# Kernel optimization log

Measured on AMD Instinct MI355X. Metric: run time of the kernel, lower is better.

Reference implementation:

```python
import jax, jax.numpy as jnp
import numpy as np

N = 100000      # nodes
E = 1600000     # edges (avg degree 16)
IN_C = 128
HID = 64
OUT_C = 2


def compute_norm(edge_index, n):
    """1/rowcount of M = I + A^T (distinct nonzeros per row, coalesce semantics)."""
    idt = edge_index.dtype
    ar = jnp.arange(n, dtype=idt)
    rows = jnp.concatenate([ar, edge_index[1]])  # M built from transposed edges
    cols = jnp.concatenate([ar, edge_index[0]])
    order = jnp.lexsort((cols, rows))
    rs, cs = rows[order], cols[order]
    uniq = jnp.concatenate([jnp.array([True]),
                            (rs[1:] != rs[:-1]) | (cs[1:] != cs[:-1])])
    rowcount = jnp.zeros((n,), jnp.float32).at[rs].add(uniq.astype(jnp.float32))
    return 1.0 / jnp.maximum(rowcount, 1.0)


def pan_conv(x, edge_index, w_lin, b_lin, w_pan, norm):
    # PyG PANConv, filter_size=1: out = diag(norm) @ (w0*I + w0*w1*A^T) @ (x W + b)
    h = x @ w_lin + b_lin                                   # [N, HID]
    src, dst = edge_index[0], edge_index[1]
    agg = jnp.zeros_like(h).at[dst].add(h[src])             # (A^T h)[i] = sum_{src->i} h[src]
    out = w_pan[0] * h + (w_pan[0] * w_pan[1]) * agg
    return norm[:, None] * out


def setup_inputs() -> dict:
    key = jax.random.key(0)
    ks = jax.random.split(key, 8)
    x = jax.random.normal(ks[0], (N, IN_C), jnp.float32)
    edge_index = jax.random.randint(ks[1], (2, E), 0, N, dtype=jnp.int32)
    w1_lin = jax.random.normal(ks[2], (IN_C, HID), jnp.float32) * 0.05
    b1_lin = jnp.zeros((HID,), jnp.float32)
    w1_pan = jax.random.uniform(ks[3], (2,), jnp.float32, 0.5, 1.5)
    w2_lin = jax.random.normal(ks[4], (HID, HID), jnp.float32) * 0.05
    b2_lin = jnp.zeros((HID,), jnp.float32)
    w2_pan = jax.random.uniform(ks[5], (2,), jnp.float32, 0.5, 1.5)
    wc = jax.random.normal(ks[6], (2 * HID, OUT_C), jnp.float32) * 0.05
    bc = jnp.zeros((OUT_C,), jnp.float32)
    return {"x": x, "edge_index": edge_index,
            "w1_lin": w1_lin, "b1_lin": b1_lin, "w1_pan": w1_pan,
            "w2_lin": w2_lin, "b2_lin": b2_lin, "w2_pan": w2_pan,
            "wc": wc, "bc": bc}


def reference(x, edge_index, w1_lin, b1_lin, w1_pan, w2_lin, b2_lin, w2_pan, wc, bc):
    n = x.shape[0]
    norm = compute_norm(edge_index, n)          # graph-structure only; shared by both layers
    h = pan_conv(x, edge_index, w1_lin, b1_lin, w1_pan, norm)
    h = jax.nn.relu(h)
    h = pan_conv(h, edge_index, w2_lin, b2_lin, w2_pan, norm)
    row, col = edge_index[0], edge_index[1]
    emb = jnp.concatenate([h[row], h[col]], axis=-1)  # [E, 2*HID]
    return emb @ wc + bc                               # [E, OUT_C]
```

## Files before the change

### kernel.cpp

```cpp
#include <hip/hip_runtime.h>
#include <hip/hip_bf16.h>

#define NNODES 100000
#define NEDGES 1600000
#define INC 128
#define HIDC 64
#define BSHIFT 7
#define NB ((NNODES + 127) / 128)
#define TILE 4096
#define HSLOTS 4096
#define CAP 4096
#define CAPE 4096
#define NBLK_FILL ((NEDGES + TILE - 1) / TILE)
#define NBLK_LIN ((NNODES + 63) / 64)

typedef short bf16x8 __attribute__((ext_vector_type(8)));
typedef float f32x4 __attribute__((ext_vector_type(4)));

__device__ __forceinline__ float bf2f(unsigned short h) {
    return __uint_as_float((unsigned)h << 16);
}
__device__ __forceinline__ unsigned short f2bf(float f) {
    __hip_bfloat16 h = __float2bfloat16(f);
    return *(unsigned short*)&h;
}

__global__ __launch_bounds__(256) void prep_w_kernel(
        const float* __restrict__ w1, unsigned short* __restrict__ wTh,
        unsigned short* __restrict__ wTl,
        const float* __restrict__ w2_lin, const float* __restrict__ b2,
        const float* __restrict__ wc, float* __restrict__ w44,
        float* __restrict__ bias4, unsigned short* __restrict__ out) {
    int t = threadIdx.x;
    int e = blockIdx.x * 256 + t;
    int c = e >> 7, k = e & 127;
    float v = w1[k * 64 + c];
    unsigned short hi = f2bf(v);
    wTh[e] = hi;
    wTl[e] = f2bf(v - bf2f(hi));
    if (blockIdx.x == 0) {
        if (t < 16)
            *(ushort4*)(out + (size_t)NNODES * 64 + t * 4) = make_ushort4(0, 0, 0, 0);
        int kk = t >> 2, j = t & 3;
        float a = 0.0f;
#pragma unroll 8
        for (int i = 0; i < 64; i++) {
            float w4 = (j < 2) ? wc[i * 2 + j] : wc[(64 + i) * 2 + (j - 2)];
            a += w2_lin[kk * 64 + i] * w4;
        }
        w44[kk * 4 + j] = a;
        if (kk == 0) {
            float bb4 = 0.0f;
            for (int i = 0; i < 64; i++) {
                float w4 = (j < 2) ? wc[i * 2 + j] : wc[(64 + i) * 2 + (j - 2)];
                bb4 += b2[i] * w4;
            }
            bias4[j] = bb4;
        }
    }
}

__global__ __launch_bounds__(256) void fat_kernel(
        const float* __restrict__ x,
        const unsigned short* __restrict__ wTh, const unsigned short* __restrict__ wTl,
        const float* __restrict__ b, unsigned short* __restrict__ out,
        const int* __restrict__ src, const int* __restrict__ dst,
        int* __restrict__ bucket_fill, unsigned int* __restrict__ staging) {
    __shared__ alignas(16) unsigned short s_a[2][64 * 128];
    __shared__ alignas(16) unsigned short s_b[2][64 * 128];
    int t = threadIdx.x;
    if (blockIdx.x < NBLK_FILL) {
        int* cnt = (int*)&s_a[0][0];
        int* basepos = cnt + NB;
        unsigned int* svl = (unsigned int*)&s_b[0][0];
        for (int i = t; i < NB; i += 256) cnt[i] = 0;
        __syncthreads();
        int tile0 = blockIdx.x * TILE;
        int meta[16];
#pragma unroll
        for (int i = 0; i < 16; i++) {
            int e = tile0 + i * 256 + t;
            meta[i] = -1;
            if (e < NEDGES) {
                int s = src[e], d = dst[e];
                int bkt = d >> BSHIFT;
                int r = atomicAdd(&cnt[bkt], 1);
                meta[i] = (bkt << 12) | r;
                svl[i * 256 + t] = ((unsigned)(d & 127) << 17) | (unsigned)s;
            }
        }
        __syncthreads();
        for (int i = t; i < NB; i += 256) {
            int c = cnt[i];
            int g = (c > 0) ? atomicAdd(&bucket_fill[i], c) : 0;
            basepos[i] = (i << 12) + g;
        }
        __syncthreads();
#pragma unroll
        for (int i = 0; i < 16; i++) {
            if (meta[i] >= 0) {
                int bkt = meta[i] >> 12, r = meta[i] & 4095;
                staging[basepos[bkt] + r] = svl[i * 256 + t];
            }
        }
    } else {
        int node0 = (blockIdx.x - NBLK_FILL) * 64;
        float4 vx[8];
#pragma unroll
        for (int it = 0; it < 8; it++) {
            int idx = it * 256 + t;
            int row = idx >> 5, c4 = idx & 31;
            int node = node0 + row;
            if (node < NNODES)
                vx[it] = *(const float4*)(x + (size_t)node * INC + c4 * 4);
            else
                vx[it] = make_float4(0.f, 0.f, 0.f, 0.f);
        }
        uint4 vwh[4], vwl[4];
#pragma unroll
        for (int j = 0; j < 4; j++) {
            vwh[j] = *(const uint4*)(wTh + (size_t)(j * 256 + t) * 8);
            vwl[j] = *(const uint4*)(wTl + (size_t)(j * 256 + t) * 8);
        }
#pragma unroll
        for (int it = 0; it < 8; it++) {
            int idx = it * 256 + t;
            int row = idx >> 5, c4 = idx & 31;
            ushort4 hi, lo;
            hi.x = f2bf(vx[it].x); lo.x = f2bf(vx[it].x - bf2f(hi.x));
            hi.y = f2bf(vx[it].y); lo.y = f2bf(vx[it].y - bf2f(hi.y));
            hi.z = f2bf(vx[it].z); lo.z = f2bf(vx[it].z - bf2f(hi.z));
            hi.w = f2bf(vx[it].w); lo.w = f2bf(vx[it].w - bf2f(hi.w));
            int ke = (c4 * 4) ^ ((row & 7) << 3);
            *(ushort4*)&s_a[0][row * 128 + ke] = hi;
            *(ushort4*)&s_a[1][row * 128 + ke] = lo;
        }
#pragma unroll
        for (int j = 0; j < 4; j++) {
            int idx = j * 256 + t;
            int col = idx >> 4, k0 = (idx & 15) * 8;
            int ke = k0 ^ ((col & 7) << 3);
            *(uint4*)&s_b[0][col * 128 + ke] = vwh[j];
            *(uint4*)&s_b[1][col * 128 + ke] = vwl[j];
        }
        __syncthreads();
        int l = t & 63, wv = t >> 6;
        int mr = l & 15, g = l >> 4;
        int arow = wv * 16 + mr;
        f32x4 acc[4] = {{0.f, 0.f, 0.f, 0.f}, {0.f, 0.f, 0.f, 0.f},
                        {0.f, 0.f, 0.f, 0.f}, {0.f, 0.f, 0.f, 0.f}};
#pragma unroll
        for (int ks = 0; ks < 4; ks++) {
            int k0 = ks * 32 + g * 8;
            int ko = k0 ^ ((mr & 7) << 3);
            bf16x8 ah = *(const bf16x8*)&s_a[0][arow * 128 + ko];
            bf16x8 al = *(const bf16x8*)&s_a[1][arow * 128 + ko];
#pragma unroll
            for (int cb = 0; cb < 4; cb++) {
                int bo = (cb * 16 + mr) * 128 + ko;
                bf16x8 bh = *(const bf16x8*)&s_b[0][bo];
                bf16x8 bl = *(const bf16x8*)&s_b[1][bo];
                acc[cb] = __builtin_amdgcn_mfma_f32_16x16x32_bf16(ah, bh, acc[cb], 0, 0, 0);
                acc[cb] = __builtin_amdgcn_mfma_f32_16x16x32_bf16(ah, bl, acc[cb], 0, 0, 0);
                acc[cb] = __builtin_amdgcn_mfma_f32_16x16x32_bf16(al, bh, acc[cb], 0, 0, 0);
            }
        }
#pragma unroll
        for (int cb = 0; cb < 4; cb++) {
            int col = cb * 16 + mr;
            float bb = b[col];
#pragma unroll
            for (int r = 0; r < 4; r++) {
                int node = node0 + wv * 16 + g * 4 + r;
                if (node < NNODES)
                    out[(size_t)node * 64 + col] = f2bf(acc[cb][r] + bb);
            }
        }
    }
}

__global__ __launch_bounds__(256) void fill2_kernel(
        const int* __restrict__ bucket_fill, const unsigned int* __restrict__ staging,
        int* __restrict__ csr_src, int* __restrict__ row_start,
        int* __restrict__ row_pdeg, float* __restrict__ norm, int n_nodes) {
    __shared__ int cnt[128];
    __shared__ int dcount[128];
    __shared__ int off[128];
    __shared__ int pscan[128];
    __shared__ unsigned short rank16[CAP];
    __shared__ unsigned int ht[HSLOTS];
    int t = threadIdx.x;
    int b = blockIdx.x;
    int node0 = b << BSHIFT;
    int nn = min(128, n_nodes - node0);
    if (t < 128) { cnt[t] = 0; dcount[t] = 0; }
    {
        uint4* h4 = (uint4*)ht;
        uint4 ff = make_uint4(0xFFFFFFFFu, 0xFFFFFFFFu, 0xFFFFFFFFu, 0xFFFFFFFFu);
        for (int i = t; i < HSLOTS / 4; i += 256) h4[i] = ff;
    }
    __syncthreads();
    int start = b << 12;
    int total = bucket_fill[b];
    for (int li = t; li < total; li += 256) {
        unsigned int w = staging[start + li];
        int s = (int)(w & 0x1FFFFu);
        int dl = (int)(w >> 17);
        int r = atomicAdd(&cnt[dl], 1);
        rank16[li] = (unsigned short)r;
        if (s != node0 + dl) {
            unsigned int slot = ((w * 2654435761u) >> 13) & (HSLOTS - 1);
            while (true) {
                unsigned int prev = atomicCAS(&ht[slot], 0xFFFFFFFFu, w);
                if (prev == 0xFFFFFFFFu) { atomicAdd(&dcount[dl], 1); break; }
                if (prev == w) break;
                slot = (slot + 1) & (HSLOTS - 1);
            }
        }
    }
    __syncthreads();
    int cv = 0, pv = 0;
    if (t < 128) {
        cv = cnt[t];
        pv = (cv + 7) & ~7;
        pscan[t] = pv;
    }
    __syncthreads();
    for (int o = 1; o < 128; o <<= 1) {
        int xx = (t >= o && t < 128) ? pscan[t - o] : 0;
        __syncthreads();
        if (t < 128) pscan[t] += xx;
        __syncthreads();
    }
    if (t < 128) off[t] = b * CAPE + pscan[t] - pv;
    __syncthreads();
    if (t < nn) {
        row_start[node0 + t] = off[t];
        row_pdeg[node0 + t] = pv;
        norm[node0 + t] = 1.0f / (1.0f + (float)dcount[t]);
    }
    if (t < 128)
        for (int k = cv; k < pv; k++) csr_src[off[t] + k] = n_nodes << 7;
    for (int li = t; li < total; li += 256) {
        unsigned int w = staging[start + li];
        int s = (int)(w & 0x1FFFFu);
        int dl = (int)(w >> 17);
        csr_src[off[dl] + (int)rank16[li]] = s << 7;
    }
}

__global__ void agg_h_kernel(const unsigned int* __restrict__ lin32,
                             const int* __restrict__ row_start,
                             const int* __restrict__ row_pdeg,
                             const int* __restrict__ csr_src,
                             const float* __restrict__ norm,
                             const float* __restrict__ wpan, const float* __restrict__ w44,
                             const float* __restrict__ bias4, float* __restrict__ u,
                             int n_nodes) {
    int t = threadIdx.x;
    int lane = t & 63;
    int sl = lane & 31;
    int h5 = lane >> 5;
    int quad = blockIdx.x * 4 + (t >> 6);
    if (blockIdx.x == 0 && t < 4) u[n_nodes * 4 + t] = 0.0f;
    int nX = quad * 4 + h5 * 2;
    int nY = nX + 1;
    int e0X = row_start[nX], pdX = row_pdeg[nX];
    int e0Y = row_start[nY], pdY = row_pdeg[nY];
    int pm = max(pdX, pdY);
    int pmax = max(pm, __shfl_xor(pm, 32));
    int sentB = n_nodes << 7;
    unsigned sl4 = (unsigned)sl * 4;
    const char* base8 = (const char*)lin32;
    float xL0 = 0.f, xH0 = 0.f, xL1 = 0.f, xH1 = 0.f;
    float yL0 = 0.f, yH0 = 0.f, yL1 = 0.f, yH1 = 0.f;
    for (int base = 0; base < pmax; base += 32) {
        int li = base + sl;
        int soX = (li < pdX) ? csr_src[e0X + li] : sentB;
        int soY = (li < pdY) ? csr_src[e0Y + li] : sentB;
        int m = min(32, pmax - base);
#pragma unroll
        for (int i = 0; i < 32; i += 2) {
            if (i < m) {
                int xA0 = __builtin_amdgcn_readlane(soX, i);
                int xB0 = __builtin_amdgcn_readlane(soX, 32 + i);
                int xA1 = __builtin_amdgcn_readlane(soX, i + 1);
                int xB1 = __builtin_amdgcn_readlane(soX, 33 + i);
                int yA0 = __builtin_amdgcn_readlane(soY, i);
                int yB0 = __builtin_amdgcn_readlane(soY, 32 + i);
                int yA1 = __builtin_amdgcn_readlane(soY, i + 1);
                int yB1 = __builtin_amdgcn_readlane(soY, 33 + i);
                int ox0 = h5 ? xB0 : xA0;
                int ox1 = h5 ? xB1 : xA1;
                int oy0 = h5 ? yB0 : yA0;
                int oy1 = h5 ? yB1 : yA1;
                unsigned int wx0 = *(const unsigned int*)(base8 + (unsigned)(ox0 + sl4));
                unsigned int wx1 = *(const unsigned int*)(base8 + (unsigned)(ox1 + sl4));
                unsigned int wy0 = *(const unsigned int*)(base8 + (unsigned)(oy0 + sl4));
                unsigned int wy1 = *(const unsigned int*)(base8 + (unsigned)(oy1 + sl4));
                xL0 += __uint_as_float(wx0 << 16);
                xH0 += __uint_as_float(wx0 & 0xFFFF0000u);
                xL1 += __uint_as_float(wx1 << 16);
                xH1 += __uint_as_float(wx1 & 0xFFFF0000u);
                yL0 += __uint_as_float(wy0 << 16);
                yH0 += __uint_as_float(wy0 & 0xFFFF0000u);
                yL1 += __uint_as_float(wy1 << 16);
                yH1 += __uint_as_float(wy1 & 0xFFFF0000u);
            }
        }
    }
    float aLX = xL0 + xL1, aHX = xH0 + xH1;
    float aLY = yL0 + yL1, aHY = yH0 + yH1;
    unsigned int wsX = *(const unsigned int*)(base8 + (unsigned)((nX << 7) + sl4));
    unsigned int wsY = *(const unsigned int*)(base8 + (unsigned)((nY << 7) + sl4));
    float nrX = norm[nX], nrY = norm[nY];
    float w0 = wpan[0];
    float w01 = wpan[0] * wpan[1];
    float vLX = fmaxf(nrX * (w0 * __uint_as_float(wsX << 16) + w01 * aLX), 0.0f);
    float vHX = fmaxf(nrX * (w0 * __uint_as_float(wsX & 0xFFFF0000u) + w01 * aHX), 0.0f);
    float vLY = fmaxf(nrY * (w0 * __uint_as_float(wsY << 16) + w01 * aLY), 0.0f);
    float vHY = fmaxf(nrY * (w0 * __uint_as_float(wsY & 0xFFFF0000u) + w01 * aHY), 0.0f);
    int c0 = 2 * sl;
    float4 wv0 = *(const float4*)(w44 + c0 * 4);
    float4 wv1 = *(const float4*)(w44 + (c0 + 1) * 4);
    float pX0 = vLX * wv0.x + vHX * wv1.x;
    float pX1 = vLX * wv0.y + vHX * wv1.y;
    float pX2 = vLX * wv0.z + vHX * wv1.z;
    float pX3 = vLX * wv0.w + vHX * wv1.w;
    float pY0 = vLY * wv0.x + vHY * wv1.x;
    float pY1 = vLY * wv0.y + vHY * wv1.y;
    float pY2 = vLY * wv0.z + vHY * wv1.z;
    float pY3 = vLY * wv0.w + vHY * wv1.w;
    for (int off = 16; off; off >>= 1) {
        pX0 += __shfl_xor(pX0, off);
        pX1 += __shfl_xor(pX1, off);
        pX2 += __shfl_xor(pX2, off);
        pX3 += __shfl_xor(pX3, off);
        pY0 += __shfl_xor(pY0, off);
        pY1 += __shfl_xor(pY1, off);
        pY2 += __shfl_xor(pY2, off);
        pY3 += __shfl_xor(pY3, off);
    }
    if (sl == 0) {
        float4 bb = *(const float4*)bias4;
        *(float4*)(u + nX * 4) =
            make_float4(pX0 + bb.x, pX1 + bb.y, pX2 + bb.z, pX3 + bb.w);
    }
    if (sl == 1) {
        float4 bb = *(const float4*)bias4;
        *(float4*)(u + nY * 4) =
            make_float4(pY0 + bb.x, pY1 + bb.y, pY2 + bb.z, pY3 + bb.w);
    }
}

__global__ void agg_pq4_kernel(const float* __restrict__ u, const int* __restrict__ row_start,
                               const int* __restrict__ row_pdeg,
                               const int* __restrict__ csr_src,
                               const float* __restrict__ norm,
                               const float* __restrict__ wpan, float* __restrict__ pq,
                               int n_nodes) {
    int t = threadIdx.x;
    int node = blockIdx.x * 64 + (t >> 2);
    int j = t & 3;
    if (node >= n_nodes) return;
    int e0 = row_start[node];
    int pd = row_pdeg[node];
    float acc = 0.0f;
    for (int e = 0; e < pd; e += 8) {
#pragma unroll
        for (int k = 0; k < 8; k++) {
            int so = csr_src[e0 + e + k];
            acc += u[(so >> 5) + j];
        }
    }
    float w0 = wpan[0];
    float w01 = wpan[0] * wpan[1];
    pq[node * 4 + j] = norm[node] * (w0 * u[node * 4 + j] + w01 * acc);
}

__global__ void edge_out_kernel(const int* __restrict__ src, const int* __restrict__ dst,
                                const float* __restrict__ pq, const float* __restrict__ bc,
                                float* __restrict__ out, int n_edges) {
    int e = blockIdx.x * blockDim.x + threadIdx.x;
    if (e >= n_edges) return;
    int r = src[e], c = dst[e];
    float2 p = *(const float2*)(pq + r * 4);
    float2 q = *(const float2*)(pq + c * 4 + 2);
    float2 o = make_float2(p.x + q.x + bc[0], p.y + q.y + bc[1]);
    *(float2*)(out + e * 2) = o;
}

extern "C" void kernel_launch(void* const* d_in, const int* in_sizes, int n_in,
                              void* d_out, int out_size, void* d_ws, size_t ws_size,
                              hipStream_t stream) {
    const float* x      = (const float*)d_in[0];
    const int*   eidx   = (const int*)d_in[1];
    const float* w1_lin = (const float*)d_in[2];
    const float* b1_lin = (const float*)d_in[3];
    const float* w1_pan = (const float*)d_in[4];
    const float* w2_lin = (const float*)d_in[5];
    const float* b2_lin = (const float*)d_in[6];
    const float* w2_pan = (const float*)d_in[7];
    const float* wc     = (const float*)d_in[8];
    const float* bc     = (const float*)d_in[9];
    float* out = (float*)d_out;

    const int* src = eidx;
    const int* dst = eidx + NEDGES;

    char* ws = (char*)d_ws;
    size_t off = 0;
    auto carve = [&](size_t bytes) {
        char* p = ws + off;
        off = (off + bytes + 255) & ~(size_t)255;
        return p;
    };
    int*   bucket_fill = (int*)carve((size_t)NB * 4);
    int*   row_start = (int*)carve((size_t)NNODES * 4);
    int*   row_pdeg  = (int*)carve((size_t)NNODES * 4);
    unsigned int* staging = (unsigned int*)carve((size_t)NB * CAP * 4);
    int*   csr_src  = (int*)carve(((size_t)NB * CAPE + 256) * 4);
    float* nrm      = (float*)carve((size_t)NNODES * 4);
    unsigned short* bufA = (unsigned short*)carve((size_t)(NNODES + 1) * HIDC * 2);
    float* u        = (float*)carve((size_t)(NNODES + 1) * 4 * 4);
    float* pq       = (float*)carve((size_t)NNODES * 4 * 4);
    float* w44      = (float*)carve((size_t)64 * 4 * 4);
    float* bias4    = (float*)carve((size_t)4 * 4);
    unsigned short* wTh = (unsigned short*)carve((size_t)HIDC * INC * 2);
    unsigned short* wTl = (unsigned short*)carve((size_t)HIDC * INC * 2);
    (void)ws_size; (void)in_sizes; (void)n_in; (void)out_size;

    hipMemsetAsync(bucket_fill, 0, (size_t)NB * 4, stream);

    prep_w_kernel<<<32, 256, 0, stream>>>(w1_lin, wTh, wTl, w2_lin, b2_lin, wc,
                                          w44, bias4, bufA);

    fat_kernel<<<NBLK_FILL + NBLK_LIN, 256, 0, stream>>>(
        x, wTh, wTl, b1_lin, bufA, src, dst, bucket_fill, staging);

    fill2_kernel<<<NB, 256, 0, stream>>>(bucket_fill, staging, csr_src, row_start, row_pdeg,
                                         nrm, NNODES);

    agg_h_kernel<<<(NNODES / 16), 256, 0, stream>>>(
        (const unsigned int*)bufA, row_start, row_pdeg, csr_src, nrm, w1_pan, w44, bias4,
        u, NNODES);

    agg_pq4_kernel<<<(NNODES + 63) / 64, 256, 0, stream>>>(
        u, row_start, row_pdeg, csr_src, nrm, w2_pan, pq, NNODES);

    edge_out_kernel<<<NEDGES / 256, 256, 0, stream>>>(src, dst, pq, bc, out, NEDGES);
}
```

Before: 233.0 us.

## Load GEMM operands directly from global memory and shrink fat kernel LDS

The linear-layer branch of the fused kernel no longer stages x and the split-bf16 weights through shared memory. Each lane now reads its MFMA fragments straight from global memory (x rows and the pre-split weight tiles) and does the hi/lo bf16 split in registers. This removes one barrier. Shared memory now holds only the edge-bucketing arrays, which cuts the per-block LDS footprint, and launch bounds ask for 5 blocks per CU to raise occupancy. The cost is uncoalesced, repeated global and L2 reads of the weights across waves and blocks.

```diff
diff --git a/kernel.cpp b/kernel.cpp
--- a/kernel.cpp
+++ b/kernel.cpp
@@ -60,19 +60,17 @@
     }
 }
 
-__global__ __launch_bounds__(256) void fat_kernel(
+__global__ __launch_bounds__(256, 5) void fat_kernel(
         const float* __restrict__ x,
         const unsigned short* __restrict__ wTh, const unsigned short* __restrict__ wTl,
         const float* __restrict__ b, unsigned short* __restrict__ out,
         const int* __restrict__ src, const int* __restrict__ dst,
         int* __restrict__ bucket_fill, unsigned int* __restrict__ staging) {
-    __shared__ alignas(16) unsigned short s_a[2][64 * 128];
-    __shared__ alignas(16) unsigned short s_b[2][64 * 128];
+    __shared__ int cnt[NB];
+    __shared__ int basepos[NB];
+    __shared__ unsigned int svl[TILE];
     int t = threadIdx.x;
     if (blockIdx.x < NBLK_FILL) {
-        int* cnt = (int*)&s_a[0][0];
-        int* basepos = cnt + NB;
-        unsigned int* svl = (unsigned int*)&s_b[0][0];
         for (int i = t; i < NB; i += 256) cnt[i] = 0;
         __syncthreads();
         int tile0 = blockIdx.x * TILE;
@@ -105,61 +103,34 @@
         }
     } else {
         int node0 = (blockIdx.x - NBLK_FILL) * 64;
-        float4 vx[8];
-#pragma unroll
-        for (int it = 0; it < 8; it++) {
-            int idx = it * 256 + t;
-            int row = idx >> 5, c4 = idx & 31;
-            int node = node0 + row;
-            if (node < NNODES)
-                vx[it] = *(const float4*)(x + (size_t)node * INC + c4 * 4);
-            else
-                vx[it] = make_float4(0.f, 0.f, 0.f, 0.f);
-        }
-        uint4 vwh[4], vwl[4];
-#pragma unroll
-        for (int j = 0; j < 4; j++) {
-            vwh[j] = *(const uint4*)(wTh + (size_t)(j * 256 + t) * 8);
-            vwl[j] = *(const uint4*)(wTl + (size_t)(j * 256 + t) * 8);
-        }
-#pragma unroll
-        for (int it = 0; it < 8; it++) {
-            int idx = it * 256 + t;
-            int row = idx >> 5, c4 = idx & 31;
-            ushort4 hi, lo;
-            hi.x = f2bf(vx[it].x); lo.x = f2bf(vx[it].x - bf2f(hi.x));
-            hi.y = f2bf(vx[it].y); lo.y = f2bf(vx[it].y - bf2f(hi.y));
-            hi.z = f2bf(vx[it].z); lo.z = f2bf(vx[it].z - bf2f(hi.z));
-            hi.w = f2bf(vx[it].w); lo.w = f2bf(vx[it].w - bf2f(hi.w));
-            int ke = (c4 * 4) ^ ((row & 7) << 3);
-            *(ushort4*)&s_a[0][row * 128 + ke] = hi;
-            *(ushort4*)&s_a[1][row * 128 + ke] = lo;
-        }
-#pragma unroll
-        for (int j = 0; j < 4; j++) {
-            int idx = j * 256 + t;
-            int col = idx >> 4, k0 = (idx & 15) * 8;
-            int ke = k0 ^ ((col & 7) << 3);
-            *(uint4*)&s_b[0][col * 128 + ke] = vwh[j];
-            *(uint4*)&s_b[1][col * 128 + ke] = vwl[j];
-        }
-        __syncthreads();
         int l = t & 63, wv = t >> 6;
         int mr = l & 15, g = l >> 4;
         int arow = wv * 16 + mr;
+        int node = node0 + arow;
+        bool vr = (node < NNODES);
+        const float* xr = x + (size_t)node * INC;
         f32x4 acc[4] = {{0.f, 0.f, 0.f, 0.f}, {0.f, 0.f, 0.f, 0.f},
                         {0.f, 0.f, 0.f, 0.f}, {0.f, 0.f, 0.f, 0.f}};
 #pragma unroll
         for (int ks = 0; ks < 4; ks++) {
             int k0 = ks * 32 + g * 8;
-            int ko = k0 ^ ((mr & 7) << 3);
-            bf16x8 ah = *(const bf16x8*)&s_a[0][arow * 128 + ko];
-            bf16x8 al = *(const bf16x8*)&s_a[1][arow * 128 + ko];
+            float4 xa = vr ? *(const float4*)(xr + k0)
+                           : make_float4(0.f, 0.f, 0.f, 0.f);
+            float4 xb = vr ? *(const float4*)(xr + k0 + 4)
+                           : make_float4(0.f, 0.f, 0.f, 0.f);
+            float xv[8] = {xa.x, xa.y, xa.z, xa.w, xb.x, xb.y, xb.z, xb.w};
+            bf16x8 ah, al;
+#pragma unroll
+            for (int j = 0; j < 8; j++) {
+                unsigned short h = f2bf(xv[j]);
+                ah[j] = (short)h;
+                al[j] = (short)f2bf(xv[j] - bf2f(h));
+            }
 #pragma unroll
             for (int cb = 0; cb < 4; cb++) {
-                int bo = (cb * 16 + mr) * 128 + ko;
-                bf16x8 bh = *(const bf16x8*)&s_b[0][bo];
-                bf16x8 bl = *(const bf16x8*)&s_b[1][bo];
+                int col = cb * 16 + mr;
+                bf16x8 bh = *(const bf16x8*)(wTh + (size_t)col * 128 + k0);
+                bf16x8 bl = *(const bf16x8*)(wTl + (size_t)col * 128 + k0);
                 acc[cb] = __builtin_amdgcn_mfma_f32_16x16x32_bf16(ah, bh, acc[cb], 0, 0, 0);
                 acc[cb] = __builtin_amdgcn_mfma_f32_16x16x32_bf16(ah, bl, acc[cb], 0, 0, 0);
                 acc[cb] = __builtin_amdgcn_mfma_f32_16x16x32_bf16(al, bh, acc[cb], 0, 0, 0);
@@ -171,9 +142,9 @@
             float bb = b[col];
 #pragma unroll
             for (int r = 0; r < 4; r++) {
-                int node = node0 + wv * 16 + g * 4 + r;
-                if (node < NNODES)
-                    out[(size_t)node * 64 + col] = f2bf(acc[cb][r] + bb);
+                int n2 = node0 + wv * 16 + g * 4 + r;
+                if (n2 < NNODES)
+                    out[(size_t)n2 * 64 + col] = f2bf(acc[cb][r] + bb);
             }
         }
     }
```

Measured after the change: 246.4 us. +5.8%, slower.
